# Optimization experiments

Measured on AMD Instinct MI355X. Metric: run time of the kernel, lower is better.

## Reference

```python
import jax, jax.numpy as jnp
from jax import lax
import numpy as np

SEQ, IN, H, C = 8192, 256, 2048, 2


def setup_inputs() -> dict:
    key = jax.random.key(0)
    ks = jax.random.split(key, 9)
    s = 1.0 / np.sqrt(H)
    u = lambda k, shape: jax.random.uniform(k, shape, jnp.float32, -s, s)
    return {
        "x": jax.random.normal(ks[0], (SEQ, 1, IN), jnp.float32),
        "h0": jax.random.normal(ks[1], (H,), jnp.float32),
        "c0": jax.random.normal(ks[2], (H,), jnp.float32),
        "w_ih": u(ks[3], (4 * H, IN)),
        "w_hh": u(ks[4], (4 * H, H)),
        "b_ih": u(ks[5], (4 * H,)),
        "b_hh": u(ks[6], (4 * H,)),
        "w_lin": u(ks[7], (C, H)),
        "b_lin": u(ks[8], (C,)),
    }


def _lstm_last_h(xs, h0, c0, w_ih, w_hh, b_ih, b_hh):
    # Precompute input contributions for all steps in one GEMM: (SEQ, 4H)
    xg = xs @ w_ih.T + (b_ih + b_hh)

    def step(carry, xg_t):
        h, c = carry
        g = xg_t + w_hh @ h  # (4H,)
        i, f, gc, o = jnp.split(g, 4)
        i = jax.nn.sigmoid(i)
        f = jax.nn.sigmoid(f)
        gc = jnp.tanh(gc)
        o = jax.nn.sigmoid(o)
        c = f * c + i * gc
        h = o * jnp.tanh(c)
        return (h, c), None

    (h, _c), _ = lax.scan(step, (h0, c0), xg)
    return h


def reference(x, h0, c0, w_ih, w_hh, b_ih, b_hh, w_lin, b_lin):
    xs = x[:, 0, :]  # (SEQ, IN), batch dim of 1 squeezed
    h = _lstm_last_h(xs, h0, c0, w_ih, w_hh, b_ih, b_hh)  # (H,)
    logit = h @ w_lin.T + b_lin  # (C,)
    return logit[None, :]  # (1, C), matching output.squeeze(dim=1) @ linear
```

## Files before the change

kernel.cpp:

```cpp
#include <hip/hip_runtime.h>
#include <math.h>

#define SEQ   8192
#define NIN   256
#define H     2048
#define NBLK  256
#define NTHR  256

typedef unsigned long long u64;

__global__ void lstm_init(const float* __restrict__ h0, float* __restrict__ ws)
{
    const int j = threadIdx.x;
    unsigned* tags = (unsigned*)(ws + 2 * H);
    #pragma unroll
    for (int r = 0; r < 8; ++r) ws[8 * j + r] = h0[8 * j + r];
    tags[j]        = 0u;
    tags[NBLK + j] = 0xFFFFFFFFu;
}

__device__ __forceinline__ void wave_poll_tags(const u64* tp, unsigned t, int ln)
{
    const u64 want = ((u64)t << 32) | (u64)t;
    for (;;) {
        u64 a = __hip_atomic_load(tp + ln,      __ATOMIC_RELAXED, __HIP_MEMORY_SCOPE_AGENT);
        u64 b = __hip_atomic_load(tp + 64 + ln, __ATOMIC_RELAXED, __HIP_MEMORY_SCOPE_AGENT);
        if (__all((a == want) && (b == want))) break;
        __builtin_amdgcn_s_sleep(2);
    }
}

__global__ void __launch_bounds__(NTHR, 1)
lstm_persist(const float* __restrict__ x, const float* __restrict__ c0,
             const float* __restrict__ w_ih, const float* __restrict__ w_hh,
             const float* __restrict__ b_ih, const float* __restrict__ b_hh,
             const float* __restrict__ w_lin, const float* __restrict__ b_lin,
             float* __restrict__ out, float* __restrict__ ws)
{
    const int b = blockIdx.x, tid = threadIdx.x;
    const int wv = tid >> 6, ln = tid & 63;
    float*     hA    = ws;
    unsigned*  tags  = (unsigned*)(ws + 2 * H);
    const u64* tagsU = (const u64*)tags;

    __shared__ float  h_lds[H + H / 32];
    __shared__ double gsum[4][8];
    __shared__ double bias_s[4][8];
    __shared__ double red0[4], red1[4];

    if (tid < 32) {
        int g = tid >> 3, r = tid & 7;
        int R = g * H + b * 8 + r;
        bias_s[g][r] = (double)b_ih[R] + (double)b_hh[R];
    }
    double c_reg = (wv == 0 && ln < 8) ? (double)c0[b * 8 + ln] : 0.0;

    float wreg[8][32];
    float wih[8][4];
    #pragma unroll
    for (int r = 0; r < 8; ++r) {
        const int R = wv * H + b * 8 + r;
        const float4* wp = (const float4*)(w_hh + (size_t)R * H + ln * 32);
        #pragma unroll
        for (int q = 0; q < 8; ++q) ((float4*)wreg[r])[q] = wp[q];
        *(float4*)wih[r] = *(const float4*)(w_ih + (size_t)R * NIN + ln * 4);
    }
    __syncthreads();

    float4 xr = *(const float4*)(x + ln * 4);
    float4 xn = xr;

    for (int t = 0; t < SEQ; ++t) {
        const int slot = t & 1;

        if (wv == 0) wave_poll_tags(tagsU + slot * (NBLK / 2), (unsigned)t, ln);
        __syncthreads();

        {
            const u64* hp = (const u64*)(hA + slot * H) + tid * 4;
            const int base = 8 * tid + (tid >> 2);
            #pragma unroll
            for (int q = 0; q < 4; ++q) {
                u64 v = __hip_atomic_load(hp + q, __ATOMIC_RELAXED, __HIP_MEMORY_SCOPE_AGENT);
                union { u64 u; float2 f; } cv; cv.u = v;
                h_lds[base + 2 * q]     = cv.f.x;
                h_lds[base + 2 * q + 1] = cv.f.y;
            }
        }
        __syncthreads();

        if (t + 1 < SEQ) xn = *(const float4*)(x + (size_t)(t + 1) * NIN + ln * 4);

        float hbuf[32];
        {
            const float* hp = &h_lds[33 * ln];
            #pragma unroll
            for (int q = 0; q < 32; ++q) hbuf[q] = hp[q];
        }
        double acc[8];
        #pragma unroll
        for (int r = 0; r < 8; ++r)
            acc[r] = (double)wih[r][0] * (double)xr.x + (double)wih[r][1] * (double)xr.y
                   + (double)wih[r][2] * (double)xr.z + (double)wih[r][3] * (double)xr.w;
        #pragma unroll
        for (int q = 0; q < 32; ++q) {
            const double hq = (double)hbuf[q];
            #pragma unroll
            for (int r = 0; r < 8; ++r)
                acc[r] = fma((double)wreg[r][q], hq, acc[r]);
        }
        #pragma unroll
        for (int off = 32; off >= 1; off >>= 1) {
            #pragma unroll
            for (int r = 0; r < 8; ++r) acc[r] += __shfl_xor(acc[r], off, 64);
        }
        if (ln == 0) {
            #pragma unroll
            for (int r = 0; r < 8; ++r) gsum[wv][r] = acc[r];
        }
        __syncthreads();

        if (wv == 0) {
            double actv = 0.0;
            if (ln < 32) {
                const int g = ln >> 3, j = ln & 7;
                double v = gsum[g][j] + bias_s[g][j];
                actv = (g == 2) ? tanh(v) : 1.0 / (1.0 + exp(-v));
            }
            const int j = ln & 7;
            double ai = __shfl(actv, j,      64);
            double af = __shfl(actv, j + 8,  64);
            double ag = __shfl(actv, j + 16, 64);
            double ao = __shfl(actv, j + 24, 64);
            if (ln < 8) {
                double c = af * c_reg + ai * ag;
                c_reg = c;
                float hnew = (float)(ao * tanh(c));
                unsigned* dst = (unsigned*)(hA + (1 - slot) * H) + 8 * b + ln;
                __hip_atomic_store(dst, __builtin_bit_cast(unsigned, hnew),
                                   __ATOMIC_RELAXED, __HIP_MEMORY_SCOPE_AGENT);
            }
            asm volatile("s_waitcnt vmcnt(0)" ::: "memory");
            if (ln == 0)
                __hip_atomic_store(&tags[(1 - slot) * NBLK + b], (unsigned)(t + 1),
                                   __ATOMIC_RELAXED, __HIP_MEMORY_SCOPE_AGENT);
        }
        xr = xn;
    }

    if (b == 0) {
        if (wv == 0) wave_poll_tags(tagsU, (unsigned)SEQ, ln);
        __syncthreads();
        double a0 = 0., a1 = 0.;
        {
            const u64* hp = (const u64*)hA + tid * 4;
            #pragma unroll
            for (int q = 0; q < 4; ++q) {
                u64 v = __hip_atomic_load(hp + q, __ATOMIC_RELAXED, __HIP_MEMORY_SCOPE_AGENT);
                union { u64 u; float2 f; } cv; cv.u = v;
                const int k = 8 * tid + 2 * q;
                a0 = fma((double)w_lin[k],         (double)cv.f.x, a0);
                a0 = fma((double)w_lin[k + 1],     (double)cv.f.y, a0);
                a1 = fma((double)w_lin[H + k],     (double)cv.f.x, a1);
                a1 = fma((double)w_lin[H + k + 1], (double)cv.f.y, a1);
            }
        }
        #pragma unroll
        for (int off = 32; off >= 1; off >>= 1) {
            a0 += __shfl_xor(a0, off, 64);
            a1 += __shfl_xor(a1, off, 64);
        }
        if (ln == 0) { red0[wv] = a0; red1[wv] = a1; }
        __syncthreads();
        if (tid == 0) {
            out[0] = (float)(red0[0] + red0[1] + red0[2] + red0[3] + (double)b_lin[0]);
            out[1] = (float)(red1[0] + red1[1] + red1[2] + red1[3] + (double)b_lin[1]);
        }
    }
}

extern "C" void kernel_launch(void* const* d_in, const int* in_sizes, int n_in,
                              void* d_out, int out_size, void* d_ws, size_t ws_size,
                              hipStream_t stream) {
    const float* x     = (const float*)d_in[0];
    const float* h0    = (const float*)d_in[1];
    const float* c0    = (const float*)d_in[2];
    const float* w_ih  = (const float*)d_in[3];
    const float* w_hh  = (const float*)d_in[4];
    const float* b_ih  = (const float*)d_in[5];
    const float* b_hh  = (const float*)d_in[6];
    const float* w_lin = (const float*)d_in[7];
    const float* b_lin = (const float*)d_in[8];
    float* out = (float*)d_out;
    float* ws  = (float*)d_ws;

    lstm_init<<<1, NTHR, 0, stream>>>(h0, ws);
    lstm_persist<<<NBLK, NTHR, 0, stream>>>(
        x, c0, w_ih, w_hh, b_ih, b_hh, w_lin, b_lin, out, ws);
}
```

Baseline: 178.9 ms.

## Pack step tag with hidden value in 64-bit records to remove separate flag

Each block now writes its new hidden values as 64-bit records holding the step number in the high half and the float in the low half. Consumers poll these records directly until every tag matches, then read the values from the same load. This replaces the separate flag array, the store-then-wait-then-flag sequence, and one barrier per step, cutting the round trips on the critical path of the recurrence. In exchange every thread polls 8 records instead of one wave polling the flags, which adds polling traffic, and each record doubles the bytes per hidden value.

```diff
diff --git a/kernel.cpp b/kernel.cpp
--- a/kernel.cpp
+++ b/kernel.cpp
@@ -9,24 +9,16 @@
 
 typedef unsigned long long u64;
 
+
 __global__ void lstm_init(const float* __restrict__ h0, float* __restrict__ ws)
 {
-    const int j = threadIdx.x;
-    unsigned* tags = (unsigned*)(ws + 2 * H);
+    const int b = threadIdx.x;
+    u64* rec = (u64*)ws;
     #pragma unroll
-    for (int r = 0; r < 8; ++r) ws[8 * j + r] = h0[8 * j + r];
-    tags[j]        = 0u;
-    tags[NBLK + j] = 0xFFFFFFFFu;
-}
-
-__device__ __forceinline__ void wave_poll_tags(const u64* tp, unsigned t, int ln)
-{
-    const u64 want = ((u64)t << 32) | (u64)t;
-    for (;;) {
-        u64 a = __hip_atomic_load(tp + ln,      __ATOMIC_RELAXED, __HIP_MEMORY_SCOPE_AGENT);
-        u64 b = __hip_atomic_load(tp + 64 + ln, __ATOMIC_RELAXED, __HIP_MEMORY_SCOPE_AGENT);
-        if (__all((a == want) && (b == want))) break;
-        __builtin_amdgcn_s_sleep(2);
+    for (int j = 0; j < 8; ++j) {
+        unsigned hv = __builtin_bit_cast(unsigned, h0[8 * b + j]);
+        rec[j * NBLK + b]        = (u64)hv;
+        rec[2048 + j * NBLK + b] = ((u64)0xFFFFFFFFu) << 32;
     }
 }
 
@@ -39,9 +31,7 @@
 {
     const int b = blockIdx.x, tid = threadIdx.x;
     const int wv = tid >> 6, ln = tid & 63;
-    float*     hA    = ws;
-    unsigned*  tags  = (unsigned*)(ws + 2 * H);
-    const u64* tagsU = (const u64*)tags;
+    u64* rec = (u64*)ws;
 
     __shared__ float  h_lds[H + H / 32];
     __shared__ double gsum[4][8];
@@ -72,20 +62,25 @@
 
     for (int t = 0; t < SEQ; ++t) {
         const int slot = t & 1;
-
-        if (wv == 0) wave_poll_tags(tagsU + slot * (NBLK / 2), (unsigned)t, ln);
-        __syncthreads();
+        const u64* rs = rec + slot * 2048;
 
         {
-            const u64* hp = (const u64*)(hA + slot * H) + tid * 4;
+            u64 v[8];
+            for (;;) {
+                bool ok = true;
+                #pragma unroll
+                for (int j = 0; j < 8; ++j) {
+                    v[j] = __hip_atomic_load(rs + j * NBLK + tid,
+                                             __ATOMIC_RELAXED, __HIP_MEMORY_SCOPE_AGENT);
+                    ok &= ((unsigned)(v[j] >> 32) == (unsigned)t);
+                }
+                if (ok) break;
+                __builtin_amdgcn_s_sleep(2);
+            }
             const int base = 8 * tid + (tid >> 2);
             #pragma unroll
-            for (int q = 0; q < 4; ++q) {
-                u64 v = __hip_atomic_load(hp + q, __ATOMIC_RELAXED, __HIP_MEMORY_SCOPE_AGENT);
-                union { u64 u; float2 f; } cv; cv.u = v;
-                h_lds[base + 2 * q]     = cv.f.x;
-                h_lds[base + 2 * q + 1] = cv.f.y;
-            }
+            for (int j = 0; j < 8; ++j)
+                h_lds[base + j] = __builtin_bit_cast(float, (unsigned)v[j]);
         }
         __syncthreads();
 
@@ -124,8 +119,8 @@
             double actv = 0.0;
             if (ln < 32) {
                 const int g = ln >> 3, j = ln & 7;
-                double v = gsum[g][j] + bias_s[g][j];
-                actv = (g == 2) ? tanh(v) : 1.0 / (1.0 + exp(-v));
+                double vs = gsum[g][j] + bias_s[g][j];
+                actv = (g == 2) ? tanh(vs) : 1.0 / (1.0 + exp(-vs));
             }
             const int j = ln & 7;
             double ai = __shfl(actv, j,      64);
@@ -136,34 +131,35 @@
                 double c = af * c_reg + ai * ag;
                 c_reg = c;
                 float hnew = (float)(ao * tanh(c));
-                unsigned* dst = (unsigned*)(hA + (1 - slot) * H) + 8 * b + ln;
-                __hip_atomic_store(dst, __builtin_bit_cast(unsigned, hnew),
-                                   __ATOMIC_RELAXED, __HIP_MEMORY_SCOPE_AGENT);
+                u64 pv = ((u64)(unsigned)(t + 1) << 32)
+                       | (u64)__builtin_bit_cast(unsigned, hnew);
+                u64* dst = rec + (1 - slot) * 2048 + ln * NBLK + b;
+                __hip_atomic_store(dst, pv, __ATOMIC_RELAXED, __HIP_MEMORY_SCOPE_AGENT);
             }
-            asm volatile("s_waitcnt vmcnt(0)" ::: "memory");
-            if (ln == 0)
-                __hip_atomic_store(&tags[(1 - slot) * NBLK + b], (unsigned)(t + 1),
-                                   __ATOMIC_RELAXED, __HIP_MEMORY_SCOPE_AGENT);
         }
         xr = xn;
     }
 
     if (b == 0) {
-        if (wv == 0) wave_poll_tags(tagsU, (unsigned)SEQ, ln);
-        __syncthreads();
+        u64 v[8];
+        for (;;) {
+            bool ok = true;
+            #pragma unroll
+            for (int j = 0; j < 8; ++j) {
+                v[j] = __hip_atomic_load(rec + j * NBLK + tid,
+                                         __ATOMIC_RELAXED, __HIP_MEMORY_SCOPE_AGENT);
+                ok &= ((unsigned)(v[j] >> 32) == (unsigned)SEQ);
+            }
+            if (ok) break;
+            __builtin_amdgcn_s_sleep(2);
+        }
         double a0 = 0., a1 = 0.;
-        {
-            const u64* hp = (const u64*)hA + tid * 4;
-            #pragma unroll
-            for (int q = 0; q < 4; ++q) {
-                u64 v = __hip_atomic_load(hp + q, __ATOMIC_RELAXED, __HIP_MEMORY_SCOPE_AGENT);
-                union { u64 u; float2 f; } cv; cv.u = v;
-                const int k = 8 * tid + 2 * q;
-                a0 = fma((double)w_lin[k],         (double)cv.f.x, a0);
-                a0 = fma((double)w_lin[k + 1],     (double)cv.f.y, a0);
-                a1 = fma((double)w_lin[H + k],     (double)cv.f.x, a1);
-                a1 = fma((double)w_lin[H + k + 1], (double)cv.f.y, a1);
-            }
+        #pragma unroll
+        for (int j = 0; j < 8; ++j) {
+            const float hv = __builtin_bit_cast(float, (unsigned)v[j]);
+            const int k = 8 * tid + j;
+            a0 = fma((double)w_lin[k],     (double)hv, a0);
+            a1 = fma((double)w_lin[H + k], (double)hv, a1);
         }
         #pragma unroll
         for (int off = 32; off >= 1; off >>= 1) {
```

After: 249.4 ms. +39.5%, slower.

## Replicate step-completion tags across 16 copies to spread polling contention

Applied to the files above, without the earlier changes.

Each block now writes its step tag into 16 replicated tag arrays, and each polling block reads only the replica chosen by its index. This spreads the 256-block spin traffic across more cache lines so fewer pollers hit the same addresses. The h-vector load changes from per-element relaxed atomics to plain float4 loads behind an acquire fence, and the next x row is prefetched before the poll. In exchange each block issues 16 tag stores per step, and the plain loads depend on the fence for correct visibility.

```diff
diff --git a/kernel.cpp b/kernel.cpp
--- a/kernel.cpp
+++ b/kernel.cpp
@@ -6,17 +6,28 @@
 #define H     2048
 #define NBLK  256
 #define NTHR  256
+#define NREP  16
 
 typedef unsigned long long u64;
+
 
 __global__ void lstm_init(const float* __restrict__ h0, float* __restrict__ ws)
 {
-    const int j = threadIdx.x;
+    const int b = threadIdx.x;
     unsigned* tags = (unsigned*)(ws + 2 * H);
     #pragma unroll
-    for (int r = 0; r < 8; ++r) ws[8 * j + r] = h0[8 * j + r];
-    tags[j]        = 0u;
-    tags[NBLK + j] = 0xFFFFFFFFu;
+    for (int r = 0; r < 8; ++r) {
+        unsigned hv = __builtin_bit_cast(unsigned, h0[8 * b + r]);
+        __hip_atomic_store((unsigned*)ws + 8 * b + r, hv,
+                           __ATOMIC_RELAXED, __HIP_MEMORY_SCOPE_AGENT);
+    }
+    #pragma unroll
+    for (int r = 0; r < NREP; ++r) {
+        __hip_atomic_store(&tags[r * NBLK + b], 0u,
+                           __ATOMIC_RELAXED, __HIP_MEMORY_SCOPE_AGENT);
+        __hip_atomic_store(&tags[(NREP + r) * NBLK + b], 0xFFFFFFFFu,
+                           __ATOMIC_RELAXED, __HIP_MEMORY_SCOPE_AGENT);
+    }
 }
 
 __device__ __forceinline__ void wave_poll_tags(const u64* tp, unsigned t, int ln)
@@ -39,9 +50,9 @@
 {
     const int b = blockIdx.x, tid = threadIdx.x;
     const int wv = tid >> 6, ln = tid & 63;
-    float*     hA    = ws;
-    unsigned*  tags  = (unsigned*)(ws + 2 * H);
-    const u64* tagsU = (const u64*)tags;
+    float*    hA   = ws;
+    unsigned* tags = (unsigned*)(ws + 2 * H);
+    const int rep  = b & (NREP - 1);
 
     __shared__ float  h_lds[H + H / 32];
     __shared__ double gsum[4][8];
@@ -73,23 +84,24 @@
     for (int t = 0; t < SEQ; ++t) {
         const int slot = t & 1;
 
-        if (wv == 0) wave_poll_tags(tagsU + slot * (NBLK / 2), (unsigned)t, ln);
-        __syncthreads();
-
+        if (t + 1 < SEQ) xn = *(const float4*)(x + (size_t)(t + 1) * NIN + ln * 4);
+
+        if (wv == 0)
+            wave_poll_tags((const u64*)(tags + (slot * NREP + rep) * NBLK),
+                           (unsigned)t, ln);
+        __syncthreads();
+
+        __builtin_amdgcn_fence(__ATOMIC_ACQUIRE, "agent");
         {
-            const u64* hp = (const u64*)(hA + slot * H) + tid * 4;
+            const float4* hp = (const float4*)(hA + slot * H) + tid * 2;
+            float4 v0 = hp[0], v1 = hp[1];
             const int base = 8 * tid + (tid >> 2);
-            #pragma unroll
-            for (int q = 0; q < 4; ++q) {
-                u64 v = __hip_atomic_load(hp + q, __ATOMIC_RELAXED, __HIP_MEMORY_SCOPE_AGENT);
-                union { u64 u; float2 f; } cv; cv.u = v;
-                h_lds[base + 2 * q]     = cv.f.x;
-                h_lds[base + 2 * q + 1] = cv.f.y;
-            }
-        }
-        __syncthreads();
-
-        if (t + 1 < SEQ) xn = *(const float4*)(x + (size_t)(t + 1) * NIN + ln * 4);
+            h_lds[base + 0] = v0.x; h_lds[base + 1] = v0.y;
+            h_lds[base + 2] = v0.z; h_lds[base + 3] = v0.w;
+            h_lds[base + 4] = v1.x; h_lds[base + 5] = v1.y;
+            h_lds[base + 6] = v1.z; h_lds[base + 7] = v1.w;
+        }
+        __syncthreads();
 
         float hbuf[32];
         {
@@ -141,28 +153,28 @@
                                    __ATOMIC_RELAXED, __HIP_MEMORY_SCOPE_AGENT);
             }
             asm volatile("s_waitcnt vmcnt(0)" ::: "memory");
-            if (ln == 0)
-                __hip_atomic_store(&tags[(1 - slot) * NBLK + b], (unsigned)(t + 1),
+            if (ln < NREP)
+                __hip_atomic_store(&tags[((1 - slot) * NREP + ln) * NBLK + b],
+                                   (unsigned)(t + 1),
                                    __ATOMIC_RELAXED, __HIP_MEMORY_SCOPE_AGENT);
         }
         xr = xn;
     }
 
     if (b == 0) {
-        if (wv == 0) wave_poll_tags(tagsU, (unsigned)SEQ, ln);
-        __syncthreads();
+        if (wv == 0) wave_poll_tags((const u64*)tags, (unsigned)SEQ, ln);
+        __syncthreads();
+        __builtin_amdgcn_fence(__ATOMIC_ACQUIRE, "agent");
         double a0 = 0., a1 = 0.;
         {
-            const u64* hp = (const u64*)hA + tid * 4;
-            #pragma unroll
-            for (int q = 0; q < 4; ++q) {
-                u64 v = __hip_atomic_load(hp + q, __ATOMIC_RELAXED, __HIP_MEMORY_SCOPE_AGENT);
-                union { u64 u; float2 f; } cv; cv.u = v;
-                const int k = 8 * tid + 2 * q;
-                a0 = fma((double)w_lin[k],         (double)cv.f.x, a0);
-                a0 = fma((double)w_lin[k + 1],     (double)cv.f.y, a0);
-                a1 = fma((double)w_lin[H + k],     (double)cv.f.x, a1);
-                a1 = fma((double)w_lin[H + k + 1], (double)cv.f.y, a1);
+            const float4* hp = (const float4*)hA + tid * 2;
+            float4 v0 = hp[0], v1 = hp[1];
+            const float hv[8] = { v0.x, v0.y, v0.z, v0.w, v1.x, v1.y, v1.z, v1.w };
+            #pragma unroll
+            for (int q = 0; q < 8; ++q) {
+                const int k = 8 * tid + q;
+                a0 = fma((double)w_lin[k],     (double)hv[q], a0);
+                a1 = fma((double)w_lin[H + k], (double)hv[q], a1);
             }
         }
         #pragma unroll
```

Result: slower. 216.5 ms (+21.0%).

## Replicate h buffers and flag arrays to spread polling contention

Applied to the files above, without the earlier changes.

Each block now writes its new hidden values to 4 replicas of the h buffer and its step tag to 16 replicas of the tag array. Readers poll and load from a replica chosen by block index, so fewer blocks hammer the same cache lines during the grid-wide barrier. The next-step x load is also moved ahead of the poll so its latency overlaps the wait. The cost is more atomic stores per step from the writer wave, plus a larger workspace footprint.

```diff
diff --git a/kernel.cpp b/kernel.cpp
--- a/kernel.cpp
+++ b/kernel.cpp
@@ -1,22 +1,36 @@
 #include <hip/hip_runtime.h>
 #include <math.h>
 
-#define SEQ   8192
-#define NIN   256
-#define H     2048
-#define NBLK  256
-#define NTHR  256
+#define SEQ    8192
+#define NIN    256
+#define H      2048
+#define NBLK   256
+#define NTHR   256
+#define NREP   16
+#define NHREP  4
 
 typedef unsigned long long u64;
+
 
 __global__ void lstm_init(const float* __restrict__ h0, float* __restrict__ ws)
 {
-    const int j = threadIdx.x;
-    unsigned* tags = (unsigned*)(ws + 2 * H);
+    const int b = threadIdx.x;
+    unsigned* tags = (unsigned*)(ws + 2 * NHREP * H);
     #pragma unroll
-    for (int r = 0; r < 8; ++r) ws[8 * j + r] = h0[8 * j + r];
-    tags[j]        = 0u;
-    tags[NBLK + j] = 0xFFFFFFFFu;
+    for (int r = 0; r < 8; ++r) {
+        unsigned hv = __builtin_bit_cast(unsigned, h0[8 * b + r]);
+        #pragma unroll
+        for (int rep = 0; rep < NHREP; ++rep)
+            __hip_atomic_store((unsigned*)ws + rep * H + 8 * b + r, hv,
+                               __ATOMIC_RELAXED, __HIP_MEMORY_SCOPE_AGENT);
+    }
+    #pragma unroll
+    for (int rep = 0; rep < NREP; ++rep) {
+        __hip_atomic_store(&tags[rep * NBLK + b], 0u,
+                           __ATOMIC_RELAXED, __HIP_MEMORY_SCOPE_AGENT);
+        __hip_atomic_store(&tags[(NREP + rep) * NBLK + b], 0xFFFFFFFFu,
+                           __ATOMIC_RELAXED, __HIP_MEMORY_SCOPE_AGENT);
+    }
 }
 
 __device__ __forceinline__ void wave_poll_tags(const u64* tp, unsigned t, int ln)
@@ -39,9 +53,11 @@
 {
     const int b = blockIdx.x, tid = threadIdx.x;
     const int wv = tid >> 6, ln = tid & 63;
-    float*     hA    = ws;
-    unsigned*  tags  = (unsigned*)(ws + 2 * H);
+    float*    hA   = ws;
+    unsigned* tags = (unsigned*)(ws + 2 * NHREP * H);
     const u64* tagsU = (const u64*)tags;
+    const int rep  = b & (NREP - 1);
+    const int hrep = b & (NHREP - 1);
 
     __shared__ float  h_lds[H + H / 32];
     __shared__ double gsum[4][8];
@@ -73,11 +89,14 @@
     for (int t = 0; t < SEQ; ++t) {
         const int slot = t & 1;
 
-        if (wv == 0) wave_poll_tags(tagsU + slot * (NBLK / 2), (unsigned)t, ln);
+        if (t + 1 < SEQ) xn = *(const float4*)(x + (size_t)(t + 1) * NIN + ln * 4);
+
+        if (wv == 0)
+            wave_poll_tags(tagsU + (slot * NREP + rep) * (NBLK / 2), (unsigned)t, ln);
         __syncthreads();
 
         {
-            const u64* hp = (const u64*)(hA + slot * H) + tid * 4;
+            const u64* hp = (const u64*)(hA + (slot * NHREP + hrep) * H) + tid * 4;
             const int base = 8 * tid + (tid >> 2);
             #pragma unroll
             for (int q = 0; q < 4; ++q) {
@@ -88,8 +107,6 @@
             }
         }
         __syncthreads();
-
-        if (t + 1 < SEQ) xn = *(const float4*)(x + (size_t)(t + 1) * NIN + ln * 4);
 
         float hbuf[32];
         {
@@ -132,17 +149,23 @@
             double af = __shfl(actv, j + 8,  64);
             double ag = __shfl(actv, j + 16, 64);
             double ao = __shfl(actv, j + 24, 64);
+            float hnewf = 0.0f;
             if (ln < 8) {
                 double c = af * c_reg + ai * ag;
                 c_reg = c;
-                float hnew = (float)(ao * tanh(c));
-                unsigned* dst = (unsigned*)(hA + (1 - slot) * H) + 8 * b + ln;
-                __hip_atomic_store(dst, __builtin_bit_cast(unsigned, hnew),
+                hnewf = (float)(ao * tanh(c));
+            }
+            float hb = __shfl(hnewf, ln & 7, 64);
+            if (ln < 8 * NHREP) {
+                unsigned* dst = (unsigned*)(hA + ((1 - slot) * NHREP + (ln >> 3)) * H)
+                              + 8 * b + (ln & 7);
+                __hip_atomic_store(dst, __builtin_bit_cast(unsigned, hb),
                                    __ATOMIC_RELAXED, __HIP_MEMORY_SCOPE_AGENT);
             }
             asm volatile("s_waitcnt vmcnt(0)" ::: "memory");
-            if (ln == 0)
-                __hip_atomic_store(&tags[(1 - slot) * NBLK + b], (unsigned)(t + 1),
+            if (ln < NREP)
+                __hip_atomic_store(&tags[((1 - slot) * NREP + ln) * NBLK + b],
+                                   (unsigned)(t + 1),
                                    __ATOMIC_RELAXED, __HIP_MEMORY_SCOPE_AGENT);
         }
         xr = xn;
```

Result: slower. 196.5 ms (+9.9%).
